# Performance work log

Hardware: AMD Instinct MI355X
Metric: run time of the kernel (lower is better)

The kernel has to match this reference:

```python
import jax, jax.numpy as jnp
import numpy as np
import math

INC, OUTC, NPARAM = 64, 128, 8
B, D, H, W = 2, 12, 48, 48
BN_EPS = 1e-5


def _p_n(num_param):
    # replicates LDConv_3D._get_p_n kernel-point layout
    base = round(math.sqrt(num_param))
    dep = round(num_param ** (1.0 / 3.0))
    row = num_param // (base * dep)
    mod = num_param % (base * dep)
    z, x, y = np.meshgrid(np.arange(dep), np.arange(row), np.arange(base), indexing='ij')
    z, x, y = z.ravel(), x.ravel(), y.ravel()
    if mod > 0:
        mz, mx, my = np.meshgrid(np.arange(dep, dep + 1), np.arange(row, row + 1), np.arange(mod), indexing='ij')
        z = np.concatenate([z, mz.ravel()])
        x = np.concatenate([x, mx.ravel()])
        y = np.concatenate([y, my.ravel()])
    return (jnp.asarray(z, jnp.float32), jnp.asarray(x, jnp.float32), jnp.asarray(y, jnp.float32))


def _conv3d(x, w, stride, pad):
    return jax.lax.conv_general_dilated(x, w, window_strides=stride, padding=pad,
                                        dimension_numbers=('NCDHW', 'OIDHW', 'NCDHW'))


def setup_inputs() -> dict:
    key = jax.random.key(0)
    ks = jax.random.split(key, 5)
    x = jax.random.normal(ks[0], (B, INC, D, H, W), jnp.float32)
    w_p = jax.random.normal(ks[1], (3 * NPARAM, INC, 3, 3, 3), jnp.float32) * 0.01
    b_p = jax.random.normal(ks[2], (3 * NPARAM,), jnp.float32) * 0.01
    w_conv = jax.random.normal(ks[3], (OUTC, INC, NPARAM, 1, 1), jnp.float32) * (1.0 / math.sqrt(INC * NPARAM))
    gamma = jnp.ones((OUTC,), jnp.float32)
    beta = jnp.zeros((OUTC,), jnp.float32)
    return {'x': x, 'w_p': w_p, 'b_p': b_p, 'w_conv': w_conv, 'gamma': gamma, 'beta': beta}


def reference(x, w_p, b_p, w_conv, gamma, beta):
    b, c, d, h, w = x.shape
    N = NPARAM
    # learned offsets: (b, 3N, d, h, w)
    offset = _conv3d(x, w_p, (1, 1, 1), [(1, 1), (1, 1), (1, 1)]) + b_p[None, :, None, None, None]
    off = jnp.transpose(offset, (0, 2, 3, 4, 1))  # b d h w 3N
    oz, ox, oy = off[..., :N], off[..., N:2 * N], off[..., 2 * N:]
    pnz, pnx, pny = _p_n(N)
    # sampling positions p = p_0 + p_n + offset  (stride=1)
    pz = oz + jnp.arange(d, dtype=jnp.float32)[None, :, None, None, None] + pnz
    px = ox + jnp.arange(h, dtype=jnp.float32)[None, None, :, None, None] + pnx
    py = oy + jnp.arange(w, dtype=jnp.float32)[None, None, None, :, None] + pny
    # integer corner coords (detached floor, clamped)
    fz = jnp.floor(jax.lax.stop_gradient(pz))
    fx = jnp.floor(jax.lax.stop_gradient(px))
    fy = jnp.floor(jax.lax.stop_gradient(py))
    qltz = jnp.clip(fz, 0, d - 1)
    qltx = jnp.clip(fx, 0, h - 1)
    qlty = jnp.clip(fy, 0, w - 1)
    qrbz = jnp.clip(fz + 1, 0, d - 1)
    qrbx = jnp.clip(fx + 1, 0, h - 1)
    qrby = jnp.clip(fy + 1, 0, w - 1)
    # clamped continuous positions
    pzc = jnp.clip(pz, 0, d - 1)
    pxc = jnp.clip(px, 0, h - 1)
    pyc = jnp.clip(py, 0, w - 1)
    # trilinear weights for the 4 gathered corners (as in source)
    g_lt = (1 + (qltz - pzc)) * (1 + (qltx - pxc)) * (1 + (qlty - pyc))
    g_rb = (1 - (qrbz - pzc)) * (1 - (qrbx - pxc)) * (1 - (qrby - pyc))
    g_lb = (1 + (qltz - pzc)) * (1 - (qrbx - pxc)) * (1 + (qlty - pyc))
    g_rt = (1 - (qrbz - pzc)) * (1 + (qltx - pxc)) * (1 - (qrby - pyc))
    x_flat = x.reshape(b, c, d * h * w)
    def gath(qz, qx, qy):
        idx = (qz.astype(jnp.int32) * (h * w) + qx.astype(jnp.int32) * w + qy.astype(jnp.int32)).reshape(b, -1)
        g = jax.vmap(lambda xf, i: jnp.take(xf, i, axis=1))(x_flat, idx)
        return g.reshape(b, c, d, h, w, N)
    x_lt = gath(qltz, qltx, qlty)
    x_rb = gath(qrbz, qrbx, qrby)
    x_lb = gath(qltz, qrbx, qlty)
    x_rt = gath(qrbz, qltx, qrby)
    x_off = (g_lt[:, None] * x_lt + g_rb[:, None] * x_rb +
             g_lb[:, None] * x_lb + g_rt[:, None] * x_rt)  # b c d h w N
    # rearrange 'b c d h w n -> b c (d n) h w'
    x_off = jnp.transpose(x_off, (0, 1, 2, 5, 3, 4)).reshape(b, c, d * N, h, w)
    out = _conv3d(x_off, w_conv, (N, 1, 1), [(0, 0), (0, 0), (0, 0)])  # b outc d h w
    # BatchNorm3d (training-mode batch stats, biased var) + SiLU
    mean = jnp.mean(out, axis=(0, 2, 3, 4), keepdims=True)
    var = jnp.mean((out - mean) ** 2, axis=(0, 2, 3, 4), keepdims=True)
    out = (out - mean) * jax.lax.rsqrt(var + BN_EPS)
    out = out * gamma[None, :, None, None, None] + beta[None, :, None, None, None]
    return jax.nn.silu(out)
```

## Files before the change

kernel.cpp:

```cpp
#include <hip/hip_runtime.h>
#include <math.h>

#define BATCH 2
#define INC   64
#define OUTCH 128
#define NP    8
#define DD    12
#define HH    48
#define WW    48
#define HW    (HH*WW)
#define DHW   (DD*HW)
#define SPTS  (BATCH*DHW)
#define KDIM  (INC*NP)
#define NELEM (BATCH*OUTCH*DHW)
#define VSTRIDE 520

#define WS_W2B  0
#define WS_W3   32768
#define WS_PART 88064
#define WS_XT   90112
#define WS_OFF  1859584

typedef __attribute__((ext_vector_type(8))) short short8;
typedef __attribute__((ext_vector_type(4))) float floatx4;

__device__ __forceinline__ ushort f2bf(float f) {
    unsigned u = __float_as_uint(f);
    unsigned r = (u + 0x7fffu + ((u >> 16) & 1u)) >> 16;
    return (ushort)r;
}

__device__ __forceinline__ unsigned interp2(unsigned a, unsigned b, unsigned c, unsigned d,
                                            float g0, float g1, float g2, float g3) {
    float vl = g0 * __uint_as_float(a << 16) + g1 * __uint_as_float(b << 16)
             + g2 * __uint_as_float(c << 16) + g3 * __uint_as_float(d << 16);
    float vh = g0 * __uint_as_float(a & 0xffff0000u) + g1 * __uint_as_float(b & 0xffff0000u)
             + g2 * __uint_as_float(c & 0xffff0000u) + g3 * __uint_as_float(d & 0xffff0000u);
    return (unsigned)f2bf(vl) | ((unsigned)f2bf(vh) << 16);
}

__global__ __launch_bounds__(256) void k_prep_w2b(const float* __restrict__ wc,
                                                  ushort* __restrict__ w2b) {
    int t = blockIdx.x * 256 + threadIdx.x;
    int j  = t & 7;
    int oc = (t >> 3) & 127;
    int kq = t >> 10;
    int e  = kq * 8 + j;
    int ic = e & 63;
    int n  = e >> 6;
    w2b[t] = f2bf(wc[(oc * INC + ic) * NP + n]);
}

__global__ __launch_bounds__(256) void k_prep_w3(const float* __restrict__ wp,
                                                 float* __restrict__ w3c) {
    int t = blockIdx.x * 256 + threadIdx.x;
    int ch = t & 31;
    int iu = t >> 5;
    w3c[t] = (ch < 24) ? wp[ch * 1728 + iu] : 0.f;
}

__global__ __launch_bounds__(256) void k_transpose_x(const float* __restrict__ x,
                                                     unsigned* __restrict__ xTu) {
    int t = blockIdx.x * 256 + threadIdx.x;
    int icp = t & 31;
    int sg  = t >> 5;
    int b   = sg / DHW;
    int s   = sg - b * DHW;
    const float* xb = x + (size_t)b * INC * DHW + s;
    float v0 = xb[(2 * icp) * DHW];
    float v1 = xb[(2 * icp + 1) * DHW];
    xTu[t] = (unsigned)f2bf(v0) | ((unsigned)f2bf(v1) << 16);
}

__global__ __launch_bounds__(256, 4) void k_conv(const float* __restrict__ x,
                                                 const float* __restrict__ w3c,
                                                 const float* __restrict__ bp,
                                                 float* __restrict__ off) {
    int t    = threadIdx.x;
    int lane = t & 63;
    int wv   = t >> 6;
    int hg   = __builtin_amdgcn_readfirstlane(wv & 1);
    int pg   = wv >> 1;
    int q0 = blockIdx.x * 128;
    int bb = q0 / DHW;
    int pt = pg * 64 + lane;
    int sp = q0 + pt - bb * DHW;
    int dp = sp / HW; int rp = sp - dp * HW; int hp = rp / WW; int wp2 = rp - hp * WW;
    const float* xb = x + (size_t)bb * INC * DHW;
    const float* wbase = w3c + hg * 12;

    float acc[12];
    #pragma unroll
    for (int c = 0; c < 12; ++c) acc[c] = bp[hg * 12 + c];

    #pragma unroll 1
    for (int kz = 0; kz < 3; ++kz) {
        int z = dp + kz - 1; bool zi = (unsigned)z < DD; int zc = zi ? z : (z < 0 ? 0 : DD - 1);
        int   addr9[9];
        float msk9[9];
        {
            int u = 0;
            #pragma unroll
            for (int kx = 0; kx < 3; ++kx) {
                int xx = hp + kx - 1; bool xi = (unsigned)xx < HH; int xc2 = xi ? xx : (xx < 0 ? 0 : HH - 1);
                #pragma unroll
                for (int ky = 0; ky < 3; ++ky) {
                    int yy = wp2 + ky - 1; bool yi = (unsigned)yy < WW; int yc = yi ? yy : (yy < 0 ? 0 : WW - 1);
                    addr9[u] = zc * HW + xc2 * WW + yc;
                    msk9[u]  = (zi && xi && yi) ? 1.f : 0.f;
                    ++u;
                }
            }
        }
        #pragma unroll 2
        for (int ic = 0; ic < 64; ++ic) {
            const float* xc = xb + ic * DHW;
            const float* wk = wbase + (ic * 27 + kz * 9) * 32;
            #pragma unroll
            for (int u = 0; u < 9; ++u) {
                float xv = xc[addr9[u]] * msk9[u];
                const float* w12 = wk + u * 32;
                #pragma unroll
                for (int c = 0; c < 12; ++c) acc[c] = fmaf(xv, w12[c], acc[c]);
            }
        }
    }

    float4* op4 = reinterpret_cast<float4*>(off + (size_t)(q0 + pt) * 24 + hg * 12);
    op4[0] = make_float4(acc[0], acc[1], acc[2],  acc[3]);
    op4[1] = make_float4(acc[4], acc[5], acc[6],  acc[7]);
    op4[2] = make_float4(acc[8], acc[9], acc[10], acc[11]);
}

__global__ __launch_bounds__(256, 4) void k_fused(const unsigned* __restrict__ xTu,
                                                  const float* __restrict__ off,
                                                  const ushort* __restrict__ w2b,
                                                  float* __restrict__ out) {
    __shared__ __align__(16) ushort sVb[32 * VSTRIDE];
    __shared__ int   sMi[4][256];
    __shared__ float sMg[4][256];
    __shared__ __align__(16) unsigned stgBuf[64 * 36];

    int t  = threadIdx.x;
    int q0 = blockIdx.x * 32;
    int bb = q0 / DHW;

    {
        int i = t >> 3, n = t & 7;
        int s = q0 + i - bb * DHW;
        int d = s / HW; int r = s - d * HW; int h = r / WW; int w = r - h * WW;

        const float* op = off + (size_t)(q0 + i) * 24;
        float a0 = op[n];
        float a1 = op[8 + n];
        float a2 = op[16 + n];

        float pnz = (n < 6) ? (float)(n / 3) : 2.f;
        float pnx = (n < 6) ? 0.f : 1.f;
        float pny = (n < 6) ? (float)(n % 3) : (float)(n - 6);
        float pz = a0 + (float)d + pnz;
        float px = a1 + (float)h + pnx;
        float py = a2 + (float)w + pny;
        float fz = floorf(pz), fx = floorf(px), fy = floorf(py);
        float z0 = fminf(fmaxf(fz, 0.f), DD - 1.f), z1 = fminf(fmaxf(fz + 1.f, 0.f), DD - 1.f);
        float x0 = fminf(fmaxf(fx, 0.f), HH - 1.f), x1 = fminf(fmaxf(fx + 1.f, 0.f), HH - 1.f);
        float y0 = fminf(fmaxf(fy, 0.f), WW - 1.f), y1 = fminf(fmaxf(fy + 1.f, 0.f), WW - 1.f);
        float pzc = fminf(fmaxf(pz, 0.f), DD - 1.f);
        float pxc = fminf(fmaxf(px, 0.f), HH - 1.f);
        float pyc = fminf(fmaxf(py, 0.f), WW - 1.f);
        float wz0 = 1.f + z0 - pzc, wz1 = 1.f - z1 + pzc;
        float wx0 = 1.f + x0 - pxc, wx1 = 1.f - x1 + pxc;
        float wy0 = 1.f + y0 - pyc, wy1 = 1.f - y1 + pyc;
        float c0 = wz0 * wy0, c1 = wz1 * wy1;
        int iz0 = (int)z0, iz1 = (int)z1, ix0 = (int)x0, ix1 = (int)x1, iy0 = (int)y0, iy1 = (int)y1;
        sMi[0][t] = (iz0 * HH + ix0) * WW + iy0;
        sMi[1][t] = (iz0 * HH + ix1) * WW + iy0;
        sMi[2][t] = (iz1 * HH + ix0) * WW + iy1;
        sMi[3][t] = (iz1 * HH + ix1) * WW + iy1;
        sMg[0][t] = c0 * wx0;
        sMg[1][t] = c0 * wx1;
        sMg[2][t] = c1 * wx0;
        sMg[3][t] = c1 * wx1;
    }
    __syncthreads();

    {
        const unsigned* xTb = xTu + (size_t)bb * DHW * 32;
        unsigned* sVbU = reinterpret_cast<unsigned*>(sVb);
        int c  = t >> 3, o = t & 7;
        int tk = t >> 4, chq = t & 15;

        #pragma unroll 1
        for (int cc = 0; cc < 16; ++cc) {
            #pragma unroll
            for (int r2 = 0; r2 < 2; ++r2) {
                int cl  = r2 * 32 + c;
                int gt  = cc * 16 + (cl >> 2);
                int cid = cl & 3;
                int idx = sMi[cid][gt];
                uint4 v = reinterpret_cast<const uint4*>(xTb + (size_t)idx * 32)[o];
                *reinterpret_cast<uint4*>(&stgBuf[cl * 36 + o * 4]) = v;
            }
            __syncthreads();
            {
                int gt = cc * 16 + tk;
                float g0 = sMg[0][gt], g1 = sMg[1][gt], g2 = sMg[2][gt], g3 = sMg[3][gt];
                uint2 A = *reinterpret_cast<const uint2*>(&stgBuf[(tk * 4 + 0) * 36 + chq * 2]);
                uint2 B = *reinterpret_cast<const uint2*>(&stgBuf[(tk * 4 + 1) * 36 + chq * 2]);
                uint2 C = *reinterpret_cast<const uint2*>(&stgBuf[(tk * 4 + 2) * 36 + chq * 2]);
                uint2 D = *reinterpret_cast<const uint2*>(&stgBuf[(tk * 4 + 3) * 36 + chq * 2]);
                unsigned o0 = interp2(A.x, B.x, C.x, D.x, g0, g1, g2, g3);
                unsigned o1 = interp2(A.y, B.y, C.y, D.y, g0, g1, g2, g3);
                int ii = gt >> 3, nn = gt & 7;
                int wb = ii * (VSTRIDE / 2) + nn * 32 + chq * 2;
                sVbU[wb]     = o0;
                sVbU[wb + 1] = o1;
            }
            __syncthreads();
        }
    }

    {
        int lane = t & 63;
        int wid  = t >> 6;
        int l16  = lane & 15;
        int q    = lane >> 4;
        int ocA0 = (wid * 2) * 16 + l16;
        const ushort* A0 = w2b + ((q * 128) + ocA0) * 8;
        const ushort* A1 = A0 + 16 * 8;
        const ushort* B0 = sVb + l16 * VSTRIDE + q * 8;
        const ushort* B1 = B0 + 16 * VSTRIDE;

        floatx4 c00 = {0.f, 0.f, 0.f, 0.f};
        floatx4 c01 = {0.f, 0.f, 0.f, 0.f};
        floatx4 c10 = {0.f, 0.f, 0.f, 0.f};
        floatx4 c11 = {0.f, 0.f, 0.f, 0.f};

        #pragma unroll 4
        for (int kt = 0; kt < 16; ++kt) {
            short8 af0 = *reinterpret_cast<const short8*>(A0 + kt * 4096);
            short8 af1 = *reinterpret_cast<const short8*>(A1 + kt * 4096);
            short8 bf0 = *reinterpret_cast<const short8*>(B0 + kt * 32);
            short8 bf1 = *reinterpret_cast<const short8*>(B1 + kt * 32);
            c00 = __builtin_amdgcn_mfma_f32_16x16x32_bf16(af0, bf0, c00, 0, 0, 0);
            c01 = __builtin_amdgcn_mfma_f32_16x16x32_bf16(af0, bf1, c01, 0, 0, 0);
            c10 = __builtin_amdgcn_mfma_f32_16x16x32_bf16(af1, bf0, c10, 0, 0, 0);
            c11 = __builtin_amdgcn_mfma_f32_16x16x32_bf16(af1, bf1, c11, 0, 0, 0);
        }

        int s0 = q0 - bb * DHW;
        float* outb = out + (size_t)bb * OUTCH * DHW + s0;
        int ocRow = (wid * 2) * 16 + q * 4;
        #pragma unroll
        for (int rg = 0; rg < 4; ++rg) {
            outb[(ocRow + rg) * DHW + l16]            = c00[rg];
            outb[(ocRow + rg) * DHW + 16 + l16]       = c01[rg];
            outb[(ocRow + 16 + rg) * DHW + l16]       = c10[rg];
            outb[(ocRow + 16 + rg) * DHW + 16 + l16]  = c11[rg];
        }
    }
}

__global__ __launch_bounds__(256) void k_stats_partial(const float* __restrict__ out,
                                                       float* __restrict__ part) {
    int c = blockIdx.x >> 3;
    int j = blockIdx.x & 7;
    int b = j & 1, quarter = j >> 1;
    const float4* p = reinterpret_cast<const float4*>(
        out + (size_t)(b * OUTCH + c) * DHW + quarter * (DHW / 4));
    float sum = 0.f, ss = 0.f;
    for (int s = threadIdx.x; s < DHW / 16; s += 256) {
        float4 v = p[s];
        sum += v.x + v.y + v.z + v.w;
        ss = fmaf(v.x, v.x, ss); ss = fmaf(v.y, v.y, ss);
        ss = fmaf(v.z, v.z, ss); ss = fmaf(v.w, v.w, ss);
    }
    __shared__ float r1[256], r2[256];
    r1[threadIdx.x] = sum; r2[threadIdx.x] = ss;
    __syncthreads();
    for (int ofs = 128; ofs > 0; ofs >>= 1) {
        if (threadIdx.x < ofs) {
            r1[threadIdx.x] += r1[threadIdx.x + ofs];
            r2[threadIdx.x] += r2[threadIdx.x + ofs];
        }
        __syncthreads();
    }
    if (threadIdx.x == 0) {
        part[c * 8 + j]             = r1[0];
        part[OUTCH * 8 + c * 8 + j] = r2[0];
    }
}

__global__ __launch_bounds__(256) void k_bn_silu(float* __restrict__ out,
                                                 const float* __restrict__ part,
                                                 const float* __restrict__ gamma,
                                                 const float* __restrict__ beta) {
    int t = blockIdx.x * 256 + threadIdx.x;
    int base = t * 4;
    int c = (base / DHW) & 127;
    float sum = 0.f, ss = 0.f;
    #pragma unroll
    for (int j = 0; j < 8; ++j) {
        sum += part[c * 8 + j];
        ss  += part[OUTCH * 8 + c * 8 + j];
    }
    const float inv_n = 1.f / (float)(BATCH * DHW);
    float mean = sum * inv_n;
    float var  = ss * inv_n - mean * mean;
    float sc   = gamma[c] * rsqrtf(var + 1e-5f);
    float bi   = beta[c] - mean * sc;
    float4 v = *reinterpret_cast<float4*>(&out[base]);
    float y0 = fmaf(v.x, sc, bi);
    float y1 = fmaf(v.y, sc, bi);
    float y2 = fmaf(v.z, sc, bi);
    float y3 = fmaf(v.w, sc, bi);
    v.x = y0 / (1.f + expf(-y0));
    v.y = y1 / (1.f + expf(-y1));
    v.z = y2 / (1.f + expf(-y2));
    v.w = y3 / (1.f + expf(-y3));
    *reinterpret_cast<float4*>(&out[base]) = v;
}

extern "C" void kernel_launch(void* const* d_in, const int* in_sizes, int n_in,
                              void* d_out, int out_size, void* d_ws, size_t ws_size,
                              hipStream_t stream) {
    const float* x     = (const float*)d_in[0];
    const float* wp    = (const float*)d_in[1];
    const float* bp    = (const float*)d_in[2];
    const float* wc    = (const float*)d_in[3];
    const float* gamma = (const float*)d_in[4];
    const float* beta  = (const float*)d_in[5];
    float* out = (float*)d_out;
    float* ws  = (float*)d_ws;

    ushort*   w2b  = reinterpret_cast<ushort*>(ws + WS_W2B);
    float*    w3c  = ws + WS_W3;
    float*    part = ws + WS_PART;
    unsigned* xTu  = reinterpret_cast<unsigned*>(ws + WS_XT);
    float*    off  = ws + WS_OFF;

    k_prep_w2b<<<65536 / 256, 256, 0, stream>>>(wc, w2b);
    k_prep_w3<<<55296 / 256, 256, 0, stream>>>(wp, w3c);
    k_conv<<<SPTS / 128, 256, 0, stream>>>(x, w3c, bp, off);
    k_transpose_x<<<(SPTS * 32) / 256, 256, 0, stream>>>(x, xTu);
    k_fused<<<SPTS / 32, 256, 0, stream>>>(xTu, off, w2b, out);
    k_stats_partial<<<OUTCH * 8, 256, 0, stream>>>(out, part);
    k_bn_silu<<<(NELEM / 4) / 256, 256, 0, stream>>>(out, part, gamma, beta);
}
```

Baseline: 296.3 us.

## Stage input rows in LDS for offset conv with 64-point blocks

The offset-predicting 3x3x3 conv now uses 128-thread blocks covering 64 consecutive spatial points. For each depth tap and half of the input channels, it cooperatively loads 4 padded rows per channel into shared memory with float4 loads, zero-masking out-of-range rows and depth. Each thread then reads its 9 taps from LDS instead of scattered global loads. This aims to cut redundant global and cache traffic and address computation, at the cost of extra barriers and 24KB of LDS per block. It relies on 64 points spanning at most 2 rows within one depth slice, which holds since 48*48 is divisible by 64.

```diff
diff --git a/kernel.cpp b/kernel.cpp
--- a/kernel.cpp
+++ b/kernel.cpp
@@ -72,22 +72,42 @@
     xTu[t] = (unsigned)f2bf(v0) | ((unsigned)f2bf(v1) << 16);
 }
 
-__global__ __launch_bounds__(256, 4) void k_conv(const float* __restrict__ x,
+__global__ __launch_bounds__(128, 8) void k_conv(const float* __restrict__ x,
                                                  const float* __restrict__ w3c,
                                                  const float* __restrict__ bp,
                                                  float* __restrict__ off) {
+    __shared__ __align__(16) float sX[32 * 192];
+
     int t    = threadIdx.x;
     int lane = t & 63;
-    int wv   = t >> 6;
-    int hg   = __builtin_amdgcn_readfirstlane(wv & 1);
-    int pg   = wv >> 1;
-    int q0 = blockIdx.x * 128;
+    int hg   = __builtin_amdgcn_readfirstlane(t >> 6);
+    int q0 = blockIdx.x * 64;
     int bb = q0 / DHW;
-    int pt = pg * 64 + lane;
-    int sp = q0 + pt - bb * DHW;
-    int dp = sp / HW; int rp = sp - dp * HW; int hp = rp / WW; int wp2 = rp - hp * WW;
+    int s0 = q0 - bb * DHW;
+    int dp = s0 / HW;
+    int r0 = s0 - dp * HW;
+    int h0 = r0 / WW;
+    int rr = r0 + lane;
+    int hp = rr / WW, wp2 = rr - hp * WW;
     const float* xb = x + (size_t)bb * INC * DHW;
     const float* wbase = w3c + hg * 12;
+
+    int   a9[9];
+    float ym[3];
+    {
+        int u = 0;
+        #pragma unroll
+        for (int kx = 0; kx < 3; ++kx) {
+            int rI = hp - h0 + kx;
+            #pragma unroll
+            for (int ky = 0; ky < 3; ++ky) {
+                int yy = wp2 + ky - 1; bool yi = (unsigned)yy < WW; int yc = yi ? yy : (yy < 0 ? 0 : WW - 1);
+                a9[u] = rI * WW + yc;
+                if (kx == 0) ym[ky] = yi ? 1.f : 0.f;
+                ++u;
+            }
+        }
+    }
 
     float acc[12];
     #pragma unroll
@@ -95,38 +115,48 @@
 
     #pragma unroll 1
     for (int kz = 0; kz < 3; ++kz) {
-        int z = dp + kz - 1; bool zi = (unsigned)z < DD; int zc = zi ? z : (z < 0 ? 0 : DD - 1);
-        int   addr9[9];
-        float msk9[9];
-        {
-            int u = 0;
-            #pragma unroll
-            for (int kx = 0; kx < 3; ++kx) {
-                int xx = hp + kx - 1; bool xi = (unsigned)xx < HH; int xc2 = xi ? xx : (xx < 0 ? 0 : HH - 1);
+        int z = dp + kz - 1; bool zi = (unsigned)z < DD;
+        int zc = zi ? z : (z < 0 ? 0 : DD - 1);
+        float zmv = zi ? 1.f : 0.f;
+        const float* xzb = xb + zc * HW;
+
+        #pragma unroll 1
+        for (int h = 0; h < 2; ++h) {
+            __syncthreads();
+            #pragma unroll 1
+            for (int k = 0; k < 12; ++k) {
+                int f  = t + k * 128;
+                int r  = f / 12;
+                int c4 = f - r * 12;
+                int icL = r >> 2, rI = r & 3;
+                int xr = h0 - 1 + rI;
+                bool rvB = (unsigned)xr < HH;
+                int rc = rvB ? xr : (xr < 0 ? 0 : HH - 1);
+                float m = rvB ? zmv : 0.f;
+                const float4* src = reinterpret_cast<const float4*>(
+                    xzb + (size_t)(h * 32 + icL) * DHW + rc * WW) + c4;
+                float4 v = *src;
+                v.x *= m; v.y *= m; v.z *= m; v.w *= m;
+                *reinterpret_cast<float4*>(&sX[(icL * 4 + rI) * WW + c4 * 4]) = v;
+            }
+            __syncthreads();
+            #pragma unroll 2
+            for (int icL = 0; icL < 32; ++icL) {
+                int ic = h * 32 + icL;
+                const float* wk = wbase + (ic * 27 + kz * 9) * 32;
+                const float* sx = sX + icL * 192;
                 #pragma unroll
-                for (int ky = 0; ky < 3; ++ky) {
-                    int yy = wp2 + ky - 1; bool yi = (unsigned)yy < WW; int yc = yi ? yy : (yy < 0 ? 0 : WW - 1);
-                    addr9[u] = zc * HW + xc2 * WW + yc;
-                    msk9[u]  = (zi && xi && yi) ? 1.f : 0.f;
-                    ++u;
+                for (int u = 0; u < 9; ++u) {
+                    float xv = sx[a9[u]] * ym[u % 3];
+                    const float* w12 = wk + u * 32;
+                    #pragma unroll
+                    for (int c = 0; c < 12; ++c) acc[c] = fmaf(xv, w12[c], acc[c]);
                 }
             }
         }
-        #pragma unroll 2
-        for (int ic = 0; ic < 64; ++ic) {
-            const float* xc = xb + ic * DHW;
-            const float* wk = wbase + (ic * 27 + kz * 9) * 32;
-            #pragma unroll
-            for (int u = 0; u < 9; ++u) {
-                float xv = xc[addr9[u]] * msk9[u];
-                const float* w12 = wk + u * 32;
-                #pragma unroll
-                for (int c = 0; c < 12; ++c) acc[c] = fmaf(xv, w12[c], acc[c]);
-            }
-        }
-    }
-
-    float4* op4 = reinterpret_cast<float4*>(off + (size_t)(q0 + pt) * 24 + hg * 12);
+    }
+
+    float4* op4 = reinterpret_cast<float4*>(off + (size_t)(q0 + lane) * 24 + hg * 12);
     op4[0] = make_float4(acc[0], acc[1], acc[2],  acc[3]);
     op4[1] = make_float4(acc[4], acc[5], acc[6],  acc[7]);
     op4[2] = make_float4(acc[8], acc[9], acc[10], acc[11]);
@@ -341,7 +371,7 @@
 
     k_prep_w2b<<<65536 / 256, 256, 0, stream>>>(wc, w2b);
     k_prep_w3<<<55296 / 256, 256, 0, stream>>>(wp, w3c);
-    k_conv<<<SPTS / 128, 256, 0, stream>>>(x, w3c, bp, off);
+    k_conv<<<SPTS / 64, 128, 0, stream>>>(x, w3c, bp, off);
     k_transpose_x<<<(SPTS * 32) / 256, 256, 0, stream>>>(x, xTu);
     k_fused<<<SPTS / 32, 256, 0, stream>>>(xTu, off, w2b, out);
     k_stats_partial<<<OUTCH * 8, 256, 0, stream>>>(out, part);
```

Measured after the change: 307.0 us. 3.6% more time.

## Stage offset-conv input rows in LDS with async double-buffered loads

Applied to the files above, without the earlier changes.

The offset conv kernel now has each block handle 64 consecutive points and stage the needed x rows (4 rows, 32 channels, per z-slice half) into shared memory using global_load_lds, double-buffered across six stages. Each wave computes 6 of the 24 output channels, replacing the earlier 2 waves × 12 channels split. Blocks are remapped in an interleaved order. The intent is to replace scattered global reads of the 27-point stencil with LDS reads and to overlap loads with compute. The cost is more barriers, lower occupancy (launch bounds 2) and more LDS use.

```diff
diff --git a/kernel.cpp b/kernel.cpp
--- a/kernel.cpp
+++ b/kernel.cpp
@@ -72,64 +72,122 @@
     xTu[t] = (unsigned)f2bf(v0) | ((unsigned)f2bf(v1) << 16);
 }
 
-__global__ __launch_bounds__(256, 4) void k_conv(const float* __restrict__ x,
+__global__ __launch_bounds__(256, 2) void k_conv(const float* __restrict__ x,
                                                  const float* __restrict__ w3c,
                                                  const float* __restrict__ bp,
                                                  float* __restrict__ off) {
+    __shared__ __align__(16) float sX[2][32 * 192];
+
     int t    = threadIdx.x;
     int lane = t & 63;
     int wv   = t >> 6;
-    int hg   = __builtin_amdgcn_readfirstlane(wv & 1);
-    int pg   = wv >> 1;
-    int q0 = blockIdx.x * 128;
+    int hgq  = __builtin_amdgcn_readfirstlane(wv);
+    int b    = blockIdx.x;
+    int wg   = (b & 7) * 108 + (b >> 3);
+    int q0 = wg * 64;
     int bb = q0 / DHW;
-    int pt = pg * 64 + lane;
-    int sp = q0 + pt - bb * DHW;
-    int dp = sp / HW; int rp = sp - dp * HW; int hp = rp / WW; int wp2 = rp - hp * WW;
+    int s0 = q0 - bb * DHW;
+    int dp = s0 / HW;
+    int r0 = s0 - dp * HW;
+    int h0 = r0 / WW;
+    int rr = r0 + lane;
+    int hp = rr / WW, wp2 = rr - hp * WW;
     const float* xb = x + (size_t)bb * INC * DHW;
-    const float* wbase = w3c + hg * 12;
-
-    float acc[12];
+    const float* wbase = w3c + hgq * 6;
+
+    int   a9[9];
+    float mxy9[9];
+    {
+        int u = 0;
+        #pragma unroll
+        for (int kx = 0; kx < 3; ++kx) {
+            int xx = hp + kx - 1; bool xi = (unsigned)xx < HH;
+            int rI = hp - h0 + kx;
+            #pragma unroll
+            for (int ky = 0; ky < 3; ++ky) {
+                int yy = wp2 + ky - 1; bool yi = (unsigned)yy < WW; int yc = yi ? yy : (yy < 0 ? 0 : WW - 1);
+                a9[u]   = rI * WW + yc;
+                mxy9[u] = (xi && yi) ? 1.f : 0.f;
+                ++u;
+            }
+        }
+    }
+    int zcA, zcB, zcC; float zmA, zmC;
+    { int z = dp - 1; bool i = (unsigned)z < DD; zcA = (i ? z : 0) * HW;      zmA = i ? 1.f : 0.f; }
+    { zcB = dp * HW; }
+    { int z = dp + 1; bool i = (unsigned)z < DD; zcC = (i ? z : DD - 1) * HW; zmC = i ? 1.f : 0.f; }
+
+    int ofs[6];
     #pragma unroll
-    for (int c = 0; c < 12; ++c) acc[c] = bp[hg * 12 + c];
-
+    for (int k = 0; k < 6; ++k) {
+        int f4 = wv * 384 + k * 64 + lane;
+        int r  = f4 / 12;
+        int c4 = f4 - r * 12;
+        int icL = r >> 2, rI = r & 3;
+        int xr = h0 - 1 + rI;
+        int rc = (unsigned)xr < HH ? xr : (xr < 0 ? 0 : HH - 1);
+        ofs[k] = icL * DHW + rc * WW + c4 * 4;
+    }
+
+    float acc[6];
+    #pragma unroll
+    for (int c = 0; c < 6; ++c) acc[c] = bp[hgq * 6 + c];
+
+#define STAGE(bufI, ss) do {                                                      \
+        int kz2 = (ss) >> 1;                                                      \
+        int zofs = kz2 == 0 ? zcA : (kz2 == 1 ? zcB : zcC);                       \
+        const float* xsrc = xb + (size_t)((ss) & 1) * 32 * DHW + zofs;            \
+        float* db = &sX[bufI][wv * 1536];                                         \
+        _Pragma("unroll")                                                         \
+        for (int k = 0; k < 6; ++k)                                               \
+            __builtin_amdgcn_global_load_lds(                                     \
+                (const __attribute__((address_space(1))) void*)(xsrc + ofs[k]),   \
+                (__attribute__((address_space(3))) void*)(db + k * 256),          \
+                16, 0, 0);                                                        \
+    } while (0)
+
+    STAGE(0, 0);
     #pragma unroll 1
-    for (int kz = 0; kz < 3; ++kz) {
-        int z = dp + kz - 1; bool zi = (unsigned)z < DD; int zc = zi ? z : (z < 0 ? 0 : DD - 1);
-        int   addr9[9];
-        float msk9[9];
-        {
-            int u = 0;
-            #pragma unroll
-            for (int kx = 0; kx < 3; ++kx) {
-                int xx = hp + kx - 1; bool xi = (unsigned)xx < HH; int xc2 = xi ? xx : (xx < 0 ? 0 : HH - 1);
-                #pragma unroll
-                for (int ky = 0; ky < 3; ++ky) {
-                    int yy = wp2 + ky - 1; bool yi = (unsigned)yy < WW; int yc = yi ? yy : (yy < 0 ? 0 : WW - 1);
-                    addr9[u] = zc * HW + xc2 * WW + yc;
-                    msk9[u]  = (zi && xi && yi) ? 1.f : 0.f;
-                    ++u;
-                }
-            }
-        }
+    for (int s = 0; s < 6; ++s) {
+        int cb = s & 1;
+        if (s < 5) {
+            STAGE(cb ^ 1, s + 1);
+            asm volatile("s_waitcnt vmcnt(6)" ::: "memory");
+        } else {
+            asm volatile("s_waitcnt vmcnt(0)" ::: "memory");
+        }
+        __builtin_amdgcn_s_barrier();
+        asm volatile("" ::: "memory");
+
+        int kz = s >> 1;
+        float zmv = kz == 0 ? zmA : (kz == 1 ? 1.f : zmC);
+        float m9[9];
+        #pragma unroll
+        for (int u = 0; u < 9; ++u) m9[u] = zmv * mxy9[u];
+        int hh = s & 1;
+        const float* sx0 = &sX[cb][0];
         #pragma unroll 2
-        for (int ic = 0; ic < 64; ++ic) {
-            const float* xc = xb + ic * DHW;
+        for (int icL = 0; icL < 32; ++icL) {
+            int ic = hh * 32 + icL;
             const float* wk = wbase + (ic * 27 + kz * 9) * 32;
+            const float* sx = sx0 + icL * 192;
             #pragma unroll
             for (int u = 0; u < 9; ++u) {
-                float xv = xc[addr9[u]] * msk9[u];
-                const float* w12 = wk + u * 32;
+                float xv = sx[a9[u]] * m9[u];
+                const float* w6 = wk + u * 32;
                 #pragma unroll
-                for (int c = 0; c < 12; ++c) acc[c] = fmaf(xv, w12[c], acc[c]);
+                for (int c = 0; c < 6; ++c) acc[c] = fmaf(xv, w6[c], acc[c]);
             }
         }
-    }
-
-    float4* op4 = reinterpret_cast<float4*>(off + (size_t)(q0 + pt) * 24 + hg * 12);
-    op4[0] = make_float4(acc[0], acc[1], acc[2],  acc[3]);
-    op4[1] = make_float4(acc[4], acc[5], acc[6],  acc[7]);
-    op4[2] = make_float4(acc[8], acc[9], acc[10], acc[11]);
+        asm volatile("" ::: "memory");
+        __builtin_amdgcn_s_barrier();
+    }
+#undef STAGE
+
+    float2* op2 = reinterpret_cast<float2*>(off + (size_t)(q0 + lane) * 24 + hgq * 6);
+    op2[0] = make_float2(acc[0], acc[1]);
+    op2[1] = make_float2(acc[2], acc[3]);
+    op2[2] = make_float2(acc[4], acc[5]);
 }
 
 __global__ __launch_bounds__(256, 4) void k_fused(const unsigned* __restrict__ xTu,
@@ -341,7 +399,7 @@
 
     k_prep_w2b<<<65536 / 256, 256, 0, stream>>>(wc, w2b);
     k_prep_w3<<<55296 / 256, 256, 0, stream>>>(wp, w3c);
-    k_conv<<<SPTS / 128, 256, 0, stream>>>(x, w3c, bp, off);
+    k_conv<<<SPTS / 64, 256, 0, stream>>>(x, w3c, bp, off);
     k_transpose_x<<<(SPTS * 32) / 256, 256, 0, stream>>>(x, xTu);
     k_fused<<<SPTS / 32, 256, 0, stream>>>(xTu, off, w2b, out);
     k_stats_partial<<<OUTCH * 8, 256, 0, stream>>>(out, part);
```

After: 353.3 us. 19.2% more time.

## Compute two adjacent outputs per lane in offset conv with float2 halo loads

Applied to the files above, without the earlier changes.

The offset 3x3x3 conv kernel now has each lane compute two horizontally adjacent output points for 6 channels, instead of one point for 12 channels. Each lane loads its 3x4 input neighbourhood as nine float2 loads and reuses them across both outputs. Out-of-range z planes are skipped entirely rather than masked, and clamped row/column offsets with precomputed masks replace per-tap address math. This cuts global load instructions and address computation per FMA. In exchange, the weight loads per FMA pair change and alignment relies on the 128-point block (two rows of 48 plus a partial row) keeping float2 loads even-aligned.

```diff
diff --git a/kernel.cpp b/kernel.cpp
--- a/kernel.cpp
+++ b/kernel.cpp
@@ -78,58 +78,92 @@
                                                  float* __restrict__ off) {
     int t    = threadIdx.x;
     int lane = t & 63;
-    int wv   = t >> 6;
-    int hg   = __builtin_amdgcn_readfirstlane(wv & 1);
-    int pg   = wv >> 1;
+    int hgq  = __builtin_amdgcn_readfirstlane(t >> 6);
     int q0 = blockIdx.x * 128;
     int bb = q0 / DHW;
-    int pt = pg * 64 + lane;
-    int sp = q0 + pt - bb * DHW;
-    int dp = sp / HW; int rp = sp - dp * HW; int hp = rp / WW; int wp2 = rp - hp * WW;
+    int s0 = q0 - bb * DHW;
+    int dp = s0 / HW;
+    int rp = s0 - dp * HW + 2 * lane;
+    int hp = rp / WW;
+    int c0 = rp - hp * WW;
     const float* xb = x + (size_t)bb * INC * DHW;
-    const float* wbase = w3c + hg * 12;
-
-    float acc[12];
+    const float* wbase = w3c + hgq * 6;
+
+    int rAo = (hp > 0      ? hp - 1 : 0     ) * WW;
+    int rMo = hp * WW;
+    int rBo = (hp < HH - 1 ? hp + 1 : HH - 1) * WW;
+    int oL = (c0 > 0)  ? c0 - 2 : 0;
+    int oM = c0;
+    int oR = (c0 < 46) ? c0 + 2 : 46;
+
+    float rm0 = (hp > 0)      ? 1.f : 0.f;
+    float rm2 = (hp < HH - 1) ? 1.f : 0.f;
+    float clm = (c0 > 0)      ? 1.f : 0.f;
+    float crm = (c0 < 46)     ? 1.f : 0.f;
+    float m0[9], m1[9];
     #pragma unroll
-    for (int c = 0; c < 12; ++c) acc[c] = bp[hg * 12 + c];
+    for (int kx = 0; kx < 3; ++kx) {
+        float rmv = kx == 0 ? rm0 : (kx == 1 ? 1.f : rm2);
+        #pragma unroll
+        for (int ky = 0; ky < 3; ++ky) {
+            int u = kx * 3 + ky;
+            m0[u] = rmv * (ky == 0 ? clm : 1.f);
+            m1[u] = rmv * (ky == 2 ? crm : 1.f);
+        }
+    }
+
+    float acc[2][6];
+    #pragma unroll
+    for (int c = 0; c < 6; ++c) { acc[0][c] = bp[hgq * 6 + c]; acc[1][c] = bp[hgq * 6 + c]; }
 
     #pragma unroll 1
     for (int kz = 0; kz < 3; ++kz) {
-        int z = dp + kz - 1; bool zi = (unsigned)z < DD; int zc = zi ? z : (z < 0 ? 0 : DD - 1);
-        int   addr9[9];
-        float msk9[9];
-        {
-            int u = 0;
+        int z = dp + kz - 1;
+        if ((unsigned)z >= DD) continue;
+        const float* xz = xb + z * HW;
+        #pragma unroll 2
+        for (int ic = 0; ic < 64; ++ic) {
+            const float* xp = xz + (size_t)ic * DHW;
+            float2 LA = *reinterpret_cast<const float2*>(xp + rAo + oL);
+            float2 MA = *reinterpret_cast<const float2*>(xp + rAo + oM);
+            float2 RA = *reinterpret_cast<const float2*>(xp + rAo + oR);
+            float2 LM = *reinterpret_cast<const float2*>(xp + rMo + oL);
+            float2 MM = *reinterpret_cast<const float2*>(xp + rMo + oM);
+            float2 RM = *reinterpret_cast<const float2*>(xp + rMo + oR);
+            float2 LB = *reinterpret_cast<const float2*>(xp + rBo + oL);
+            float2 MB = *reinterpret_cast<const float2*>(xp + rBo + oM);
+            float2 RB = *reinterpret_cast<const float2*>(xp + rBo + oR);
+            const float* wk = wbase + (ic * 27 + kz * 9) * 32;
             #pragma unroll
             for (int kx = 0; kx < 3; ++kx) {
-                int xx = hp + kx - 1; bool xi = (unsigned)xx < HH; int xc2 = xi ? xx : (xx < 0 ? 0 : HH - 1);
+                float tv[4];
+                if (kx == 0)      { tv[0] = LA.y; tv[1] = MA.x; tv[2] = MA.y; tv[3] = RA.x; }
+                else if (kx == 1) { tv[0] = LM.y; tv[1] = MM.x; tv[2] = MM.y; tv[3] = RM.x; }
+                else              { tv[0] = LB.y; tv[1] = MB.x; tv[2] = MB.y; tv[3] = RB.x; }
                 #pragma unroll
                 for (int ky = 0; ky < 3; ++ky) {
-                    int yy = wp2 + ky - 1; bool yi = (unsigned)yy < WW; int yc = yi ? yy : (yy < 0 ? 0 : WW - 1);
-                    addr9[u] = zc * HW + xc2 * WW + yc;
-                    msk9[u]  = (zi && xi && yi) ? 1.f : 0.f;
-                    ++u;
+                    int u = kx * 3 + ky;
+                    const float* w6 = wk + u * 32;
+                    float xv0 = tv[ky]     * m0[u];
+                    float xv1 = tv[ky + 1] * m1[u];
+                    #pragma unroll
+                    for (int c = 0; c < 6; ++c) {
+                        acc[0][c] = fmaf(xv0, w6[c], acc[0][c]);
+                        acc[1][c] = fmaf(xv1, w6[c], acc[1][c]);
+                    }
                 }
             }
         }
-        #pragma unroll 2
-        for (int ic = 0; ic < 64; ++ic) {
-            const float* xc = xb + ic * DHW;
-            const float* wk = wbase + (ic * 27 + kz * 9) * 32;
-            #pragma unroll
-            for (int u = 0; u < 9; ++u) {
-                float xv = xc[addr9[u]] * msk9[u];
-                const float* w12 = wk + u * 32;
-                #pragma unroll
-                for (int c = 0; c < 12; ++c) acc[c] = fmaf(xv, w12[c], acc[c]);
-            }
-        }
-    }
-
-    float4* op4 = reinterpret_cast<float4*>(off + (size_t)(q0 + pt) * 24 + hg * 12);
-    op4[0] = make_float4(acc[0], acc[1], acc[2],  acc[3]);
-    op4[1] = make_float4(acc[4], acc[5], acc[6],  acc[7]);
-    op4[2] = make_float4(acc[8], acc[9], acc[10], acc[11]);
+    }
+
+    float2* o0 = reinterpret_cast<float2*>(off + (size_t)(q0 + 2 * lane) * 24 + hgq * 6);
+    o0[0] = make_float2(acc[0][0], acc[0][1]);
+    o0[1] = make_float2(acc[0][2], acc[0][3]);
+    o0[2] = make_float2(acc[0][4], acc[0][5]);
+    float2* o1 = reinterpret_cast<float2*>(off + (size_t)(q0 + 2 * lane + 1) * 24 + hgq * 6);
+    o1[0] = make_float2(acc[1][0], acc[1][1]);
+    o1[1] = make_float2(acc[1][2], acc[1][3]);
+    o1[2] = make_float2(acc[1][4], acc[1][5]);
 }
 
 __global__ __launch_bounds__(256, 4) void k_fused(const unsigned* __restrict__ xTu,
```

After: 257.8 us. 1.15x faster.
